# Performance work log

Measured on AMD Instinct MI355X. Metric: run time of the kernel, lower is better.

Reference implementation:

```python
import jax, jax.numpy as jnp
import numpy as np

N = 50000      # nodes
E = 1_600_000  # edges (avg degree 32)
G = 2000       # graphs in batch
H = 2          # attention heads
C = 64         # out_channels
IN = 64        # in_channels
NEG_SLOPE = 0.2


def setup_inputs() -> dict:
    key = jax.random.key(0)
    ks = jax.random.split(key, 6)
    x = jax.random.normal(ks[0], (N, IN), dtype=jnp.float32)
    edge_index = jax.random.randint(ks[1], (2, E), 0, N, dtype=jnp.int32)
    batch = jnp.sort(jax.random.randint(ks[2], (N,), 0, G, dtype=jnp.int32))
    # GATConv params: lin weight [H*C, IN] (glorot-ish), att vectors, bias [C]
    W = jax.random.normal(ks[3], (H * C, IN), dtype=jnp.float32) * (1.0 / np.sqrt(IN))
    att_src = jax.random.normal(ks[4], (1, H, C), dtype=jnp.float32) * 0.1
    att_dst = jax.random.normal(ks[5], (1, H, C), dtype=jnp.float32) * 0.1
    bias = jnp.zeros((C,), dtype=jnp.float32)
    return {"x": x, "edge_index": edge_index, "batch": batch,
            "W": W, "att_src": att_src, "att_dst": att_dst, "bias": bias}


def reference(x, edge_index, batch, W, att_src, att_dst, bias):
    # --- GATConv (PyG semantics: add_self_loops=True, concat=False -> head mean + bias) ---
    loops = jnp.arange(N, dtype=edge_index.dtype)
    src = jnp.concatenate([edge_index[0], loops])  # [E+N]
    dst = jnp.concatenate([edge_index[1], loops])  # [E+N]

    xp = (x @ W.T).reshape(N, H, C)                 # projected node feats [N,H,C]
    a_src = jnp.sum(xp * att_src, axis=-1)          # [N,H]
    a_dst = jnp.sum(xp * att_dst, axis=-1)          # [N,H]

    e = jax.nn.leaky_relu(a_src[src] + a_dst[dst], NEG_SLOPE)  # [E+N,H]
    # segment softmax over incoming edges of each destination node
    m = jax.ops.segment_max(e, dst, num_segments=N)            # [N,H]
    e = jnp.exp(e - m[dst])
    s = jax.ops.segment_sum(e, dst, num_segments=N)            # [N,H]
    alpha = e / s[dst]                                         # [E+N,H]

    msg = xp[src] * alpha[:, :, None]                          # [E+N,H,C]
    out = jax.ops.segment_sum(msg, dst, num_segments=N)        # [N,H,C]
    h_nodes = out.mean(axis=1) + bias                          # [N,C]

    # --- global_mean_pool ---
    sums = jax.ops.segment_sum(h_nodes, batch, num_segments=G)                     # [G,C]
    cnt = jax.ops.segment_sum(jnp.ones((N, 1), h_nodes.dtype), batch, num_segments=G)
    h_graphs = sums / jnp.maximum(cnt, 1.0)                                        # [G,C]
    return (h_nodes, h_graphs)
```

## Files before the change

### kernel.cpp

```cpp
#include <hip/hip_runtime.h>
#include <hip/hip_bf16.h>

#define H 2
#define C 64
#define IN_CH 64
#define HC (H*C)
#define NEG_SLOPE 0.2f
#define NBUCK_MAX 256
#define SBLK 512
#define CAP 12288

__global__ __launch_bounds__(128) void proj_kernel(
    const float* __restrict__ x, const float* __restrict__ W,
    const float* __restrict__ att_src, const float* __restrict__ att_dst,
    __hip_bfloat16* __restrict__ xp, float* __restrict__ asrc,
    float* __restrict__ adst, int* __restrict__ cnt, int N, int nbuck) {
    int t = threadIdx.x;
    if (blockIdx.x == 0)
        for (int i = t; i < nbuck; i += 128) cnt[i] = 0;
    float w[64];
    const float4* wr = reinterpret_cast<const float4*>(W + (size_t)t * IN_CH);
#pragma unroll
    for (int q = 0; q < 16; q++) {
        float4 v = wr[q];
        w[4 * q] = v.x; w[4 * q + 1] = v.y; w[4 * q + 2] = v.z; w[4 * q + 3] = v.w;
    }
    float a_s = att_src[t], a_d = att_dst[t];
    int lane = t & 63, head = t >> 6;
    for (int n = blockIdx.x; n < N; n += gridDim.x) {
        const float* xr = x + (size_t)n * IN_CH;
        float acc = 0.f;
#pragma unroll
        for (int k = 0; k < 64; k++) acc = fmaf(w[k], xr[k], acc);
        xp[(size_t)n * HC + t] = __float2bfloat16(acc);
        float as = acc * a_s, ad = acc * a_d;
#pragma unroll
        for (int d = 32; d > 0; d >>= 1) {
            as += __shfl_xor(as, d, 64);
            ad += __shfl_xor(ad, d, 64);
        }
        if (lane == 0) {
            asrc[(size_t)n * H + head] = as;
            adst[(size_t)n * H + head] = ad;
        }
    }
}

__global__ __launch_bounds__(256) void scatter_kernel(
    const int* __restrict__ edge, int* __restrict__ cnt,
    int* __restrict__ staged, int N, int E) {
    const int tid = threadIdx.x, bid = blockIdx.x;
    const int nbuck = (N + 255) >> 8;
    const int chunkE = (E + SBLK - 1) / SBLK;
    const int* srcE = edge;
    const int* dstE = edge + E;
    __shared__ int lh[NBUCK_MAX], bse[NBUCK_MAX], lcur[NBUCK_MAX];
    for (int i = tid; i < nbuck; i += 256) { lh[i] = 0; lcur[i] = 0; }
    __syncthreads();
    int beg = bid * chunkE, end = min(beg + chunkE, E);
    for (int i = beg + tid; i < end; i += 256)
        atomicAdd(&lh[dstE[i] >> 8], 1);
    __syncthreads();
    for (int i = tid; i < nbuck; i += 256) {
        int c = lh[i];
        bse[i] = (c > 0) ? atomicAdd(&cnt[i], c) : 0;
    }
    __syncthreads();
    for (int i = beg + tid; i < end; i += 256) {
        int s = srcE[i], d = dstE[i];
        int b = d >> 8;
        int l = atomicAdd(&lcur[b], 1);
        staged[(size_t)b * CAP + bse[b] + l] = s | ((d & 255) << 20);
    }
}

__global__ __launch_bounds__(512) void bucket_csr_kernel(
    const int* __restrict__ staged, const int* __restrict__ cnt,
    int* __restrict__ off, int* __restrict__ csr, int N, int nbuck) {
    int b = blockIdx.x, t = threadIdx.x;
    __shared__ int bse[256], rs[256], lh[256], sh[256], cur[256];
    {
        int v = (t < nbuck) ? cnt[t] : 0;
        if (t < 256) { bse[t] = v; rs[t] = v; }
        __syncthreads();
        for (int d = 1; d < 256; d <<= 1) {
            int u = (t >= d && t < 256) ? bse[t - d] : 0;
            __syncthreads();
            if (t < 256) bse[t] += u;
            __syncthreads();
        }
        if (t < 256) bse[t] -= rs[t];
        __syncthreads();
    }
    int base = bse[b], size = rs[b];
    const int* st = staged + (size_t)b * CAP;
    if (t < 256) lh[t] = 0;
    __syncthreads();
    for (int i = t; i < size; i += 512)
        atomicAdd(&lh[st[i] >> 20], 1);
    __syncthreads();
    int v = (t < 256) ? lh[t] : 0;
    if (t < 256) sh[t] = v;
    __syncthreads();
    for (int d = 1; d < 256; d <<= 1) {
        int u = (t >= d && t < 256) ? sh[t - d] : 0;
        __syncthreads();
        if (t < 256) sh[t] += u;
        __syncthreads();
    }
    if (t < 256) {
        int ex = sh[t] - v;
        int nd = b * 256 + t;
        if (nd < N) off[nd] = base + ex;
        if (nd == N - 1) off[N] = base + size;
        cur[t] = base + ex;
    }
    __syncthreads();
    for (int i = t; i < size; i += 512) {
        int e = st[i];
        int pos = atomicAdd(&cur[e >> 20], 1);
        csr[pos] = e & 0xFFFFF;
    }
}

template<int NB16>
__device__ __forceinline__ void gather_fma(const uint* __restrict__ xpw,
                                           const int* __restrict__ sidx,
                                           const float2* __restrict__ swt,
                                           int lane, float& accx, float& accy) {
    uint bu[NB16 * 16];
#pragma unroll
    for (int j = 0; j < NB16 * 16; j++) {
        int s2 = sidx[j];
        bu[j] = xpw[(size_t)s2 * 64 + lane];
    }
#pragma unroll
    for (int j = 0; j < NB16 * 16; j++) {
        float2 wv = swt[j];
        float wgt = (lane < 32) ? wv.x : wv.y;
        accx = fmaf(wgt, __uint_as_float(bu[j] << 16), accx);
        accy = fmaf(wgt, __uint_as_float(bu[j] & 0xffff0000u), accy);
    }
}

__global__ __launch_bounds__(256, 4) void aggregate_kernel(
    const __hip_bfloat16* __restrict__ xp, const float2* __restrict__ asrc,
    const float2* __restrict__ adst, const int* __restrict__ off,
    const int* __restrict__ csr, const float* __restrict__ bias,
    float* __restrict__ out, int N) {
    __shared__ int sidx[4][64];
    __shared__ float2 swt[4][64];
    int wid = threadIdx.x >> 6;
    int n = blockIdx.x * 4 + wid;
    if (n >= N) return;
    int lane = threadIdx.x & 63;
    int* si = sidx[wid];
    float2* sw = swt[wid];
    int o0 = off[n];
    int degE = off[n + 1] - o0;
    float2 ad = adst[n];
    float2 asn = asrc[n];
    float es0 = asn.x + ad.x; es0 = (es0 > 0.f) ? es0 : NEG_SLOPE * es0;
    float es1 = asn.y + ad.y; es1 = (es1 > 0.f) ? es1 : NEG_SLOPE * es1;
    float ws0 = __expf(es0), ws1 = __expf(es1);
    float s0 = (lane == 0) ? ws0 : 0.f;
    float s1 = (lane == 0) ? ws1 : 0.f;

    const uint* xpw = reinterpret_cast<const uint*>(xp);
    float accx, accy;
    {
        float wgt = (lane < 32) ? ws0 : ws1;
        uint u = xpw[(size_t)n * 64 + lane];
        accx = wgt * __uint_as_float(u << 16);
        accy = wgt * __uint_as_float(u & 0xffff0000u);
    }

    for (int base = 0; base < degE; base += 64) {
        int i = base + lane;
        int idx = 0;
        float w0 = 0.f, w1 = 0.f;
        if (i < degE) {
            idx = csr[o0 + i];
            float2 as = asrc[idx];
            float t0 = as.x + ad.x; t0 = (t0 > 0.f) ? t0 : NEG_SLOPE * t0;
            float t1 = as.y + ad.y; t1 = (t1 > 0.f) ? t1 : NEG_SLOPE * t1;
            w0 = __expf(t0);
            w1 = __expf(t1);
        }
        s0 += w0;
        s1 += w1;
        si[lane] = idx;
        sw[lane] = make_float2(w0, w1);
        int cnt2 = min(degE - base, 64);
        int nb16 = (cnt2 + 15) >> 4;
        switch (nb16) {
            case 1: gather_fma<1>(xpw, si, sw, lane, accx, accy); break;
            case 2: gather_fma<2>(xpw, si, sw, lane, accx, accy); break;
            case 3: gather_fma<3>(xpw, si, sw, lane, accx, accy); break;
            default: gather_fma<4>(xpw, si, sw, lane, accx, accy); break;
        }
    }
#pragma unroll
    for (int d = 32; d > 0; d >>= 1) {
        s0 += __shfl_xor(s0, d, 64);
        s1 += __shfl_xor(s1, d, 64);
    }
    float inv = (lane < 32) ? (1.f / s0) : (1.f / s1);
    accx *= inv;
    accy *= inv;
    float ox = 0.5f * (accx + __shfl_xor(accx, 32, 64));
    float oy = 0.5f * (accy + __shfl_xor(accy, 32, 64));
    if (lane < 32) {
        float vx = ox + bias[2 * lane];
        float vy = oy + bias[2 * lane + 1];
        *reinterpret_cast<float2*>(out + (size_t)n * C + 2 * lane) = make_float2(vx, vy);
    }
}

__global__ __launch_bounds__(256) void pool_kernel(const float* __restrict__ hn,
                                                   const int* __restrict__ batch,
                                                   float* __restrict__ outG, int N, int G) {
    int g = blockIdx.x;
    int c = threadIdx.x & 63, r = threadIdx.x >> 6;
    int lo = 0, hi = N;
    while (lo < hi) { int mid = (lo + hi) >> 1; if (batch[mid] < g) lo = mid + 1; else hi = mid; }
    int beg = lo;
    hi = N;
    while (lo < hi) { int mid = (lo + hi) >> 1; if (batch[mid] <= g) lo = mid + 1; else hi = mid; }
    int end = lo;
    float s = 0.f;
    for (int n = beg + r; n < end; n += 4) s += hn[(size_t)n * C + c];
    __shared__ float red[256];
    red[threadIdx.x] = s;
    __syncthreads();
    if (r == 0) {
        float tot = red[c] + red[64 + c] + red[128 + c] + red[192 + c];
        outG[(size_t)g * C + c] = tot / fmaxf((float)(end - beg), 1.f);
    }
}

extern "C" void kernel_launch(void* const* d_in, const int* in_sizes, int n_in,
                              void* d_out, int out_size, void* d_ws, size_t ws_size,
                              hipStream_t stream) {
    const float* x       = (const float*)d_in[0];
    const int*   edge    = (const int*)d_in[1];
    const int*   batch   = (const int*)d_in[2];
    const float* W       = (const float*)d_in[3];
    const float* att_src = (const float*)d_in[4];
    const float* att_dst = (const float*)d_in[5];
    const float* bias    = (const float*)d_in[6];

    int N = in_sizes[0] / IN_CH;
    int E = in_sizes[1] / 2;
    int G = out_size / C - N;
    int nbuck = (N + 255) >> 8;

    char* p = (char*)d_ws;
    auto alloc = [&](size_t bytes) {
        char* r = p;
        p += (bytes + 255) & ~(size_t)255;
        return r;
    };
    __hip_bfloat16* xp = (__hip_bfloat16*)alloc((size_t)N * HC * 2);
    float* asrc    = (float*)alloc((size_t)N * H * 4);
    float* adst    = (float*)alloc((size_t)N * H * 4);
    int*   cnt     = (int*)alloc((size_t)nbuck * 4);
    int*   off     = (int*)alloc((size_t)(N + 1) * 4);
    int*   staged  = (int*)alloc((size_t)nbuck * CAP * 4);
    int*   csr     = (int*)alloc((size_t)E * 4);

    proj_kernel<<<2048, 128, 0, stream>>>(x, W, att_src, att_dst, xp, asrc, adst,
                                          cnt, N, nbuck);
    scatter_kernel<<<SBLK, 256, 0, stream>>>(edge, cnt, staged, N, E);
    bucket_csr_kernel<<<nbuck, 512, 0, stream>>>(staged, cnt, off, csr, N, nbuck);
    aggregate_kernel<<<(N + 3) / 4, 256, 0, stream>>>(xp, (const float2*)asrc,
                                                      (const float2*)adst, off, csr, bias,
                                                      (float*)d_out, N);
    pool_kernel<<<G, 256, 0, stream>>>((const float*)d_out, batch,
                                       (float*)d_out + (size_t)N * C, N, G);
}
```

Before: 215.4 us.

## Fuse bucket CSR build into aggregation kernel using LDS-resident adjacency

Removes the separate bucket_csr kernel and the global off/csr arrays. Each aggregation block now reads one staged bucket, keeps only the destination nodes of its quarter, counting-sorts their sources into LDS and aggregates 64 nodes (16 per wave). This cuts a kernel launch and the global CSR write and read. In exchange each bucket's staged edges are read four times, and the grid shrinks to about 784 blocks of 256 threads with 16KB of LDS each, which may reduce occupancy and latency hiding for the gathers.

```diff
diff --git a/kernel.cpp b/kernel.cpp
--- a/kernel.cpp
+++ b/kernel.cpp
@@ -9,6 +9,7 @@
 #define NBUCK_MAX 256
 #define SBLK 512
 #define CAP 12288
+#define QCAP 4096
 
 __global__ __launch_bounds__(128) void proj_kernel(
     const float* __restrict__ x, const float* __restrict__ W,
@@ -74,55 +75,6 @@
     }
 }
 
-__global__ __launch_bounds__(512) void bucket_csr_kernel(
-    const int* __restrict__ staged, const int* __restrict__ cnt,
-    int* __restrict__ off, int* __restrict__ csr, int N, int nbuck) {
-    int b = blockIdx.x, t = threadIdx.x;
-    __shared__ int bse[256], rs[256], lh[256], sh[256], cur[256];
-    {
-        int v = (t < nbuck) ? cnt[t] : 0;
-        if (t < 256) { bse[t] = v; rs[t] = v; }
-        __syncthreads();
-        for (int d = 1; d < 256; d <<= 1) {
-            int u = (t >= d && t < 256) ? bse[t - d] : 0;
-            __syncthreads();
-            if (t < 256) bse[t] += u;
-            __syncthreads();
-        }
-        if (t < 256) bse[t] -= rs[t];
-        __syncthreads();
-    }
-    int base = bse[b], size = rs[b];
-    const int* st = staged + (size_t)b * CAP;
-    if (t < 256) lh[t] = 0;
-    __syncthreads();
-    for (int i = t; i < size; i += 512)
-        atomicAdd(&lh[st[i] >> 20], 1);
-    __syncthreads();
-    int v = (t < 256) ? lh[t] : 0;
-    if (t < 256) sh[t] = v;
-    __syncthreads();
-    for (int d = 1; d < 256; d <<= 1) {
-        int u = (t >= d && t < 256) ? sh[t - d] : 0;
-        __syncthreads();
-        if (t < 256) sh[t] += u;
-        __syncthreads();
-    }
-    if (t < 256) {
-        int ex = sh[t] - v;
-        int nd = b * 256 + t;
-        if (nd < N) off[nd] = base + ex;
-        if (nd == N - 1) off[N] = base + size;
-        cur[t] = base + ex;
-    }
-    __syncthreads();
-    for (int i = t; i < size; i += 512) {
-        int e = st[i];
-        int pos = atomicAdd(&cur[e >> 20], 1);
-        csr[pos] = e & 0xFFFFF;
-    }
-}
-
 template<int NB16>
 __device__ __forceinline__ void gather_fma(const uint* __restrict__ xpw,
                                            const int* __restrict__ sidx,
@@ -143,77 +95,115 @@
     }
 }
 
-__global__ __launch_bounds__(256, 4) void aggregate_kernel(
+__global__ __launch_bounds__(256, 4) void csr_aggregate_kernel(
+    const int* __restrict__ staged, const int* __restrict__ cnt,
     const __hip_bfloat16* __restrict__ xp, const float2* __restrict__ asrc,
-    const float2* __restrict__ adst, const int* __restrict__ off,
-    const int* __restrict__ csr, const float* __restrict__ bias,
+    const float2* __restrict__ adst, const float* __restrict__ bias,
     float* __restrict__ out, int N) {
-    __shared__ int sidx[4][64];
+    int b = blockIdx.x >> 2, q = blockIdx.x & 3;
+    int tid = threadIdx.x, lane = tid & 63, wid = tid >> 6;
+    __shared__ int lh[64], sc[64], cur[64];
+    __shared__ int ldsCsr[QCAP];
     __shared__ float2 swt[4][64];
-    int wid = threadIdx.x >> 6;
-    int n = blockIdx.x * 4 + wid;
-    if (n >= N) return;
-    int lane = threadIdx.x & 63;
-    int* si = sidx[wid];
-    float2* sw = swt[wid];
-    int o0 = off[n];
-    int degE = off[n + 1] - o0;
-    float2 ad = adst[n];
-    float2 asn = asrc[n];
-    float es0 = asn.x + ad.x; es0 = (es0 > 0.f) ? es0 : NEG_SLOPE * es0;
-    float es1 = asn.y + ad.y; es1 = (es1 > 0.f) ? es1 : NEG_SLOPE * es1;
-    float ws0 = __expf(es0), ws1 = __expf(es1);
-    float s0 = (lane == 0) ? ws0 : 0.f;
-    float s1 = (lane == 0) ? ws1 : 0.f;
+    int size = cnt[b];
+    const int* st = staged + (size_t)b * CAP;
+
+    if (tid < 64) lh[tid] = 0;
+    __syncthreads();
+    for (int i = tid; i < size; i += 256) {
+        int e = st[i];
+        int dl = e >> 20;
+        if ((dl >> 6) == q) atomicAdd(&lh[dl & 63], 1);
+    }
+    __syncthreads();
+    if (tid < 64) {
+        int v = lh[tid];
+        int incl = v;
+#pragma unroll
+        for (int d = 1; d < 64; d <<= 1) {
+            int u = __shfl_up(incl, d, 64);
+            if (lane >= d) incl += u;
+        }
+        sc[tid] = incl - v;
+        cur[tid] = incl - v;
+    }
+    __syncthreads();
+    int total = sc[63] + lh[63];
+    for (int i = tid; i < size; i += 256) {
+        int e = st[i];
+        int dl = e >> 20;
+        if ((dl >> 6) == q) {
+            int pos = atomicAdd(&cur[dl & 63], 1);
+            ldsCsr[pos] = e & 0xFFFFF;
+        }
+    }
+    __syncthreads();
+    if (tid < 80) {
+        int z = total + tid;
+        if (z < QCAP) ldsCsr[z] = 0;
+    }
+    __syncthreads();
 
     const uint* xpw = reinterpret_cast<const uint*>(xp);
-    float accx, accy;
-    {
-        float wgt = (lane < 32) ? ws0 : ws1;
-        uint u = xpw[(size_t)n * 64 + lane];
-        accx = wgt * __uint_as_float(u << 16);
-        accy = wgt * __uint_as_float(u & 0xffff0000u);
-    }
-
-    for (int base = 0; base < degE; base += 64) {
-        int i = base + lane;
-        int idx = 0;
-        float w0 = 0.f, w1 = 0.f;
-        if (i < degE) {
-            idx = csr[o0 + i];
-            float2 as = asrc[idx];
-            float t0 = as.x + ad.x; t0 = (t0 > 0.f) ? t0 : NEG_SLOPE * t0;
-            float t1 = as.y + ad.y; t1 = (t1 > 0.f) ? t1 : NEG_SLOPE * t1;
-            w0 = __expf(t0);
-            w1 = __expf(t1);
-        }
-        s0 += w0;
-        s1 += w1;
-        si[lane] = idx;
-        sw[lane] = make_float2(w0, w1);
-        int cnt2 = min(degE - base, 64);
-        int nb16 = (cnt2 + 15) >> 4;
-        switch (nb16) {
-            case 1: gather_fma<1>(xpw, si, sw, lane, accx, accy); break;
-            case 2: gather_fma<2>(xpw, si, sw, lane, accx, accy); break;
-            case 3: gather_fma<3>(xpw, si, sw, lane, accx, accy); break;
-            default: gather_fma<4>(xpw, si, sw, lane, accx, accy); break;
-        }
-    }
-#pragma unroll
-    for (int d = 32; d > 0; d >>= 1) {
-        s0 += __shfl_xor(s0, d, 64);
-        s1 += __shfl_xor(s1, d, 64);
-    }
-    float inv = (lane < 32) ? (1.f / s0) : (1.f / s1);
-    accx *= inv;
-    accy *= inv;
-    float ox = 0.5f * (accx + __shfl_xor(accx, 32, 64));
-    float oy = 0.5f * (accy + __shfl_xor(accy, 32, 64));
-    if (lane < 32) {
-        float vx = ox + bias[2 * lane];
-        float vy = oy + bias[2 * lane + 1];
-        *reinterpret_cast<float2*>(out + (size_t)n * C + 2 * lane) = make_float2(vx, vy);
+    for (int k = 0; k < 16; k++) {
+        int l = wid * 16 + k;
+        int n = b * 256 + q * 64 + l;
+        if (n >= N) break;
+        int o0 = sc[l];
+        int degE = lh[l];
+        float2 ad = adst[n];
+        float2 asn = asrc[n];
+        float es0 = asn.x + ad.x; es0 = (es0 > 0.f) ? es0 : NEG_SLOPE * es0;
+        float es1 = asn.y + ad.y; es1 = (es1 > 0.f) ? es1 : NEG_SLOPE * es1;
+        float ws0 = __expf(es0), ws1 = __expf(es1);
+        float s0 = (lane == 0) ? ws0 : 0.f;
+        float s1 = (lane == 0) ? ws1 : 0.f;
+        float accx, accy;
+        {
+            float wgt = (lane < 32) ? ws0 : ws1;
+            uint u = xpw[(size_t)n * 64 + lane];
+            accx = wgt * __uint_as_float(u << 16);
+            accy = wgt * __uint_as_float(u & 0xffff0000u);
+        }
+        for (int base = 0; base < degE; base += 64) {
+            int i = base + lane;
+            float w0 = 0.f, w1 = 0.f;
+            if (i < degE) {
+                int idx = ldsCsr[o0 + i];
+                float2 as = asrc[idx];
+                float t0 = as.x + ad.x; t0 = (t0 > 0.f) ? t0 : NEG_SLOPE * t0;
+                float t1 = as.y + ad.y; t1 = (t1 > 0.f) ? t1 : NEG_SLOPE * t1;
+                w0 = __expf(t0);
+                w1 = __expf(t1);
+            }
+            s0 += w0;
+            s1 += w1;
+            swt[wid][lane] = make_float2(w0, w1);
+            int cnt2 = min(degE - base, 64);
+            int nb16 = (cnt2 + 15) >> 4;
+            const int* sidx = ldsCsr + o0 + base;
+            switch (nb16) {
+                case 1: gather_fma<1>(xpw, sidx, swt[wid], lane, accx, accy); break;
+                case 2: gather_fma<2>(xpw, sidx, swt[wid], lane, accx, accy); break;
+                case 3: gather_fma<3>(xpw, sidx, swt[wid], lane, accx, accy); break;
+                default: gather_fma<4>(xpw, sidx, swt[wid], lane, accx, accy); break;
+            }
+        }
+#pragma unroll
+        for (int d = 32; d > 0; d >>= 1) {
+            s0 += __shfl_xor(s0, d, 64);
+            s1 += __shfl_xor(s1, d, 64);
+        }
+        float inv = (lane < 32) ? (1.f / s0) : (1.f / s1);
+        accx *= inv;
+        accy *= inv;
+        float ox = 0.5f * (accx + __shfl_xor(accx, 32, 64));
+        float oy = 0.5f * (accy + __shfl_xor(accy, 32, 64));
+        if (lane < 32) {
+            float vx = ox + bias[2 * lane];
+            float vy = oy + bias[2 * lane + 1];
+            *reinterpret_cast<float2*>(out + (size_t)n * C + 2 * lane) = make_float2(vx, vy);
+        }
     }
 }
 
@@ -265,17 +255,15 @@
     float* asrc    = (float*)alloc((size_t)N * H * 4);
     float* adst    = (float*)alloc((size_t)N * H * 4);
     int*   cnt     = (int*)alloc((size_t)nbuck * 4);
-    int*   off     = (int*)alloc((size_t)(N + 1) * 4);
     int*   staged  = (int*)alloc((size_t)nbuck * CAP * 4);
-    int*   csr     = (int*)alloc((size_t)E * 4);
 
     proj_kernel<<<2048, 128, 0, stream>>>(x, W, att_src, att_dst, xp, asrc, adst,
                                           cnt, N, nbuck);
     scatter_kernel<<<SBLK, 256, 0, stream>>>(edge, cnt, staged, N, E);
-    bucket_csr_kernel<<<nbuck, 512, 0, stream>>>(staged, cnt, off, csr, N, nbuck);
-    aggregate_kernel<<<(N + 3) / 4, 256, 0, stream>>>(xp, (const float2*)asrc,
-                                                      (const float2*)adst, off, csr, bias,
-                                                      (float*)d_out, N);
+    csr_aggregate_kernel<<<nbuck * 4, 256, 0, stream>>>(staged, cnt, xp,
+                                                        (const float2*)asrc,
+                                                        (const float2*)adst, bias,
+                                                        (float*)d_out, N);
     pool_kernel<<<G, 256, 0, stream>>>((const float*)d_out, batch,
                                        (float*)d_out + (size_t)N * C, N, G);
 }
```

New measurement: 223.3 us. 3.7% more time.

## Precompute edge attention weights and softmax denominators in CSR build kernel

Applied to the files above, without the earlier changes.

Moves the per-edge leaky-relu/exp weight computation and the per-node softmax denominator out of the aggregate kernel into the CSR construction kernel, where they are written to new wts and den arrays using shared-memory atomics. The aggregate kernel then loads precomputed weights instead of gathering asrc and recomputing exp, and drops its final shuffle reduction. The gather unroll granularity also changes from 16 to 8 edges to cut wasted loads on partial chunks. The cost is an extra 8 bytes per edge written and read back, plus float atomics in shared memory in the CSR kernel.

```diff
diff --git a/kernel.cpp b/kernel.cpp
--- a/kernel.cpp
+++ b/kernel.cpp
@@ -74,11 +74,15 @@
     }
 }
 
-__global__ __launch_bounds__(512) void bucket_csr_kernel(
+__global__ __launch_bounds__(512) void csr_weights_kernel(
     const int* __restrict__ staged, const int* __restrict__ cnt,
-    int* __restrict__ off, int* __restrict__ csr, int N, int nbuck) {
+    const float2* __restrict__ asrc, const float2* __restrict__ adst,
+    int* __restrict__ off, int* __restrict__ csr, float2* __restrict__ wts,
+    float2* __restrict__ den, int N, int nbuck) {
     int b = blockIdx.x, t = threadIdx.x;
     __shared__ int bse[256], rs[256], lh[256], sh[256], cur[256];
+    __shared__ float2 adL[256];
+    __shared__ float denS[512];
     {
         int v = (t < nbuck) ? cnt[t] : 0;
         if (t < 256) { bse[t] = v; rs[t] = v; }
@@ -94,7 +98,23 @@
     }
     int base = bse[b], size = rs[b];
     const int* st = staged + (size_t)b * CAP;
-    if (t < 256) lh[t] = 0;
+    if (t < 256) {
+        lh[t] = 0;
+        int nd = b * 256 + t;
+        if (nd < N) {
+            float2 ad = adst[nd];
+            adL[t] = ad;
+            float2 asn = asrc[nd];
+            float e0 = asn.x + ad.x; e0 = (e0 > 0.f) ? e0 : NEG_SLOPE * e0;
+            float e1 = asn.y + ad.y; e1 = (e1 > 0.f) ? e1 : NEG_SLOPE * e1;
+            denS[2 * t] = __expf(e0);
+            denS[2 * t + 1] = __expf(e1);
+        } else {
+            adL[t] = make_float2(0.f, 0.f);
+            denS[2 * t] = 1.f;
+            denS[2 * t + 1] = 1.f;
+        }
+    }
     __syncthreads();
     for (int i = t; i < size; i += 512)
         atomicAdd(&lh[st[i] >> 20], 1);
@@ -118,24 +138,38 @@
     __syncthreads();
     for (int i = t; i < size; i += 512) {
         int e = st[i];
-        int pos = atomicAdd(&cur[e >> 20], 1);
-        csr[pos] = e & 0xFFFFF;
-    }
-}
-
-template<int NB16>
+        int s = e & 0xFFFFF, dl = e >> 20;
+        float2 as = asrc[s];
+        float2 ad = adL[dl];
+        float e0 = as.x + ad.x; e0 = (e0 > 0.f) ? e0 : NEG_SLOPE * e0;
+        float e1 = as.y + ad.y; e1 = (e1 > 0.f) ? e1 : NEG_SLOPE * e1;
+        float w0 = __expf(e0), w1 = __expf(e1);
+        int pos = atomicAdd(&cur[dl], 1);
+        csr[pos] = s;
+        wts[pos] = make_float2(w0, w1);
+        atomicAdd(&denS[2 * dl], w0);
+        atomicAdd(&denS[2 * dl + 1], w1);
+    }
+    __syncthreads();
+    if (t < 256) {
+        int nd = b * 256 + t;
+        if (nd < N) den[nd] = make_float2(denS[2 * t], denS[2 * t + 1]);
+    }
+}
+
+template<int NB>
 __device__ __forceinline__ void gather_fma(const uint* __restrict__ xpw,
                                            const int* __restrict__ sidx,
                                            const float2* __restrict__ swt,
                                            int lane, float& accx, float& accy) {
-    uint bu[NB16 * 16];
-#pragma unroll
-    for (int j = 0; j < NB16 * 16; j++) {
+    uint bu[NB * 8];
+#pragma unroll
+    for (int j = 0; j < NB * 8; j++) {
         int s2 = sidx[j];
         bu[j] = xpw[(size_t)s2 * 64 + lane];
     }
 #pragma unroll
-    for (int j = 0; j < NB16 * 16; j++) {
+    for (int j = 0; j < NB * 8; j++) {
         float2 wv = swt[j];
         float wgt = (lane < 32) ? wv.x : wv.y;
         accx = fmaf(wgt, __uint_as_float(bu[j] << 16), accx);
@@ -146,7 +180,8 @@
 __global__ __launch_bounds__(256, 4) void aggregate_kernel(
     const __hip_bfloat16* __restrict__ xp, const float2* __restrict__ asrc,
     const float2* __restrict__ adst, const int* __restrict__ off,
-    const int* __restrict__ csr, const float* __restrict__ bias,
+    const int* __restrict__ csr, const float2* __restrict__ wts,
+    const float2* __restrict__ den, const float* __restrict__ bias,
     float* __restrict__ out, int N) {
     __shared__ int sidx[4][64];
     __shared__ float2 swt[4][64];
@@ -158,13 +193,12 @@
     float2* sw = swt[wid];
     int o0 = off[n];
     int degE = off[n + 1] - o0;
+    float2 dn = den[n];
     float2 ad = adst[n];
     float2 asn = asrc[n];
     float es0 = asn.x + ad.x; es0 = (es0 > 0.f) ? es0 : NEG_SLOPE * es0;
     float es1 = asn.y + ad.y; es1 = (es1 > 0.f) ? es1 : NEG_SLOPE * es1;
     float ws0 = __expf(es0), ws1 = __expf(es1);
-    float s0 = (lane == 0) ? ws0 : 0.f;
-    float s1 = (lane == 0) ? ws1 : 0.f;
 
     const uint* xpw = reinterpret_cast<const uint*>(xp);
     float accx, accy;
@@ -178,34 +212,27 @@
     for (int base = 0; base < degE; base += 64) {
         int i = base + lane;
         int idx = 0;
-        float w0 = 0.f, w1 = 0.f;
+        float2 w2 = make_float2(0.f, 0.f);
         if (i < degE) {
             idx = csr[o0 + i];
-            float2 as = asrc[idx];
-            float t0 = as.x + ad.x; t0 = (t0 > 0.f) ? t0 : NEG_SLOPE * t0;
-            float t1 = as.y + ad.y; t1 = (t1 > 0.f) ? t1 : NEG_SLOPE * t1;
-            w0 = __expf(t0);
-            w1 = __expf(t1);
-        }
-        s0 += w0;
-        s1 += w1;
+            w2 = wts[o0 + i];
+        }
         si[lane] = idx;
-        sw[lane] = make_float2(w0, w1);
+        sw[lane] = w2;
         int cnt2 = min(degE - base, 64);
-        int nb16 = (cnt2 + 15) >> 4;
-        switch (nb16) {
+        int nb8 = (cnt2 + 7) >> 3;
+        switch (nb8) {
             case 1: gather_fma<1>(xpw, si, sw, lane, accx, accy); break;
             case 2: gather_fma<2>(xpw, si, sw, lane, accx, accy); break;
             case 3: gather_fma<3>(xpw, si, sw, lane, accx, accy); break;
-            default: gather_fma<4>(xpw, si, sw, lane, accx, accy); break;
-        }
-    }
-#pragma unroll
-    for (int d = 32; d > 0; d >>= 1) {
-        s0 += __shfl_xor(s0, d, 64);
-        s1 += __shfl_xor(s1, d, 64);
-    }
-    float inv = (lane < 32) ? (1.f / s0) : (1.f / s1);
+            case 4: gather_fma<4>(xpw, si, sw, lane, accx, accy); break;
+            case 5: gather_fma<5>(xpw, si, sw, lane, accx, accy); break;
+            case 6: gather_fma<6>(xpw, si, sw, lane, accx, accy); break;
+            case 7: gather_fma<7>(xpw, si, sw, lane, accx, accy); break;
+            default: gather_fma<8>(xpw, si, sw, lane, accx, accy); break;
+        }
+    }
+    float inv = (lane < 32) ? (1.f / dn.x) : (1.f / dn.y);
     accx *= inv;
     accy *= inv;
     float ox = 0.5f * (accx + __shfl_xor(accx, 32, 64));
@@ -268,14 +295,18 @@
     int*   off     = (int*)alloc((size_t)(N + 1) * 4);
     int*   staged  = (int*)alloc((size_t)nbuck * CAP * 4);
     int*   csr     = (int*)alloc((size_t)E * 4);
+    float2* wts    = (float2*)alloc((size_t)E * 8);
+    float2* den    = (float2*)alloc((size_t)N * 8);
 
     proj_kernel<<<2048, 128, 0, stream>>>(x, W, att_src, att_dst, xp, asrc, adst,
                                           cnt, N, nbuck);
     scatter_kernel<<<SBLK, 256, 0, stream>>>(edge, cnt, staged, N, E);
-    bucket_csr_kernel<<<nbuck, 512, 0, stream>>>(staged, cnt, off, csr, N, nbuck);
+    csr_weights_kernel<<<nbuck, 512, 0, stream>>>(staged, cnt, (const float2*)asrc,
+                                                  (const float2*)adst, off, csr, wts, den,
+                                                  N, nbuck);
     aggregate_kernel<<<(N + 3) / 4, 256, 0, stream>>>(xp, (const float2*)asrc,
-                                                      (const float2*)adst, off, csr, bias,
-                                                      (float*)d_out, N);
+                                                      (const float2*)adst, off, csr, wts, den,
+                                                      bias, (float*)d_out, N);
     pool_kernel<<<G, 256, 0, stream>>>((const float*)d_out, batch,
                                        (float*)d_out + (size_t)N * C, N, G);
 }
```

After: 226.7 us. +5.3%, slower.

## Fuse mean-pool into aggregation via atomics, shrink buckets, cache edges in LDS

Applied to the files above, without the earlier changes.

The per-graph mean pool now happens inside the aggregation kernel. Each node atomically adds its output row into per-graph sums and counts, and a small finalize kernel divides. This removes the separate pool kernel that re-read node outputs after a binary search. The CSR build uses 128-node buckets instead of 256, which means more bucket blocks with smaller per-bucket scans. The scatter kernel caches its edge chunk in LDS so edges are read from global memory only once. The cost is many float atomics on hot graph rows, plus float-sum ordering that is no longer deterministic.

```diff
diff --git a/kernel.cpp b/kernel.cpp
--- a/kernel.cpp
+++ b/kernel.cpp
@@ -6,18 +6,25 @@
 #define IN_CH 64
 #define HC (H*C)
 #define NEG_SLOPE 0.2f
-#define NBUCK_MAX 256
+#define NBUCK_MAX 512
 #define SBLK 512
-#define CAP 12288
+#define CHUNK_MAX 3136
+#define CAP 6144
 
 __global__ __launch_bounds__(128) void proj_kernel(
     const float* __restrict__ x, const float* __restrict__ W,
     const float* __restrict__ att_src, const float* __restrict__ att_dst,
     __hip_bfloat16* __restrict__ xp, float* __restrict__ asrc,
-    float* __restrict__ adst, int* __restrict__ cnt, int N, int nbuck) {
+    float* __restrict__ adst, int* __restrict__ cnt, float* __restrict__ gsum,
+    int* __restrict__ gcnt, int N, int nbuck, int G) {
     int t = threadIdx.x;
-    if (blockIdx.x == 0)
+    if (blockIdx.x < 64) {
+        for (int i = blockIdx.x * 128 + t; i < G * C; i += 64 * 128) gsum[i] = 0.f;
+    } else if (blockIdx.x == 64) {
+        for (int i = t; i < G; i += 128) gcnt[i] = 0;
+    } else if (blockIdx.x == 65) {
         for (int i = t; i < nbuck; i += 128) cnt[i] = 0;
+    }
     float w[64];
     const float4* wr = reinterpret_cast<const float4*>(W + (size_t)t * IN_CH);
 #pragma unroll
@@ -50,27 +57,30 @@
     const int* __restrict__ edge, int* __restrict__ cnt,
     int* __restrict__ staged, int N, int E) {
     const int tid = threadIdx.x, bid = blockIdx.x;
-    const int nbuck = (N + 255) >> 8;
+    const int nbuck = (N + 127) >> 7;
     const int chunkE = (E + SBLK - 1) / SBLK;
     const int* srcE = edge;
     const int* dstE = edge + E;
+    __shared__ int2 eds[CHUNK_MAX];
     __shared__ int lh[NBUCK_MAX], bse[NBUCK_MAX], lcur[NBUCK_MAX];
     for (int i = tid; i < nbuck; i += 256) { lh[i] = 0; lcur[i] = 0; }
     __syncthreads();
     int beg = bid * chunkE, end = min(beg + chunkE, E);
-    for (int i = beg + tid; i < end; i += 256)
-        atomicAdd(&lh[dstE[i] >> 8], 1);
-    __syncthreads();
-    for (int i = tid; i < nbuck; i += 256) {
-        int c = lh[i];
-        bse[i] = (c > 0) ? atomicAdd(&cnt[i], c) : 0;
-    }
-    __syncthreads();
-    for (int i = beg + tid; i < end; i += 256) {
-        int s = srcE[i], d = dstE[i];
-        int b = d >> 8;
+    int m = end - beg;
+    for (int i = tid; i < m; i += 256) {
+        int s = srcE[beg + i], d = dstE[beg + i];
+        eds[i] = make_int2(s, d);
+        atomicAdd(&lh[d >> 7], 1);
+    }
+    __syncthreads();
+    for (int i = tid; i < nbuck; i += 256)
+        bse[i] = atomicAdd(&cnt[i], lh[i]);
+    __syncthreads();
+    for (int i = tid; i < m; i += 256) {
+        int2 e = eds[i];
+        int b = e.y >> 7;
         int l = atomicAdd(&lcur[b], 1);
-        staged[(size_t)b * CAP + bse[b] + l] = s | ((d & 255) << 20);
+        staged[(size_t)b * CAP + bse[b] + l] = e.x | ((e.y & 127) << 20);
     }
 }
 
@@ -78,39 +88,39 @@
     const int* __restrict__ staged, const int* __restrict__ cnt,
     int* __restrict__ off, int* __restrict__ csr, int N, int nbuck) {
     int b = blockIdx.x, t = threadIdx.x;
-    __shared__ int bse[256], rs[256], lh[256], sh[256], cur[256];
+    __shared__ int bse[512], rs[512], lh[128], sh[128], cur[128];
     {
         int v = (t < nbuck) ? cnt[t] : 0;
-        if (t < 256) { bse[t] = v; rs[t] = v; }
-        __syncthreads();
-        for (int d = 1; d < 256; d <<= 1) {
-            int u = (t >= d && t < 256) ? bse[t - d] : 0;
+        bse[t] = v; rs[t] = v;
+        __syncthreads();
+        for (int d = 1; d < 512; d <<= 1) {
+            int u = (t >= d) ? bse[t - d] : 0;
             __syncthreads();
-            if (t < 256) bse[t] += u;
+            bse[t] += u;
             __syncthreads();
         }
-        if (t < 256) bse[t] -= rs[t];
+        bse[t] -= rs[t];
         __syncthreads();
     }
     int base = bse[b], size = rs[b];
     const int* st = staged + (size_t)b * CAP;
-    if (t < 256) lh[t] = 0;
+    if (t < 128) lh[t] = 0;
     __syncthreads();
     for (int i = t; i < size; i += 512)
         atomicAdd(&lh[st[i] >> 20], 1);
     __syncthreads();
-    int v = (t < 256) ? lh[t] : 0;
-    if (t < 256) sh[t] = v;
-    __syncthreads();
-    for (int d = 1; d < 256; d <<= 1) {
-        int u = (t >= d && t < 256) ? sh[t - d] : 0;
-        __syncthreads();
-        if (t < 256) sh[t] += u;
-        __syncthreads();
-    }
-    if (t < 256) {
+    int v = (t < 128) ? lh[t] : 0;
+    if (t < 128) sh[t] = v;
+    __syncthreads();
+    for (int d = 1; d < 128; d <<= 1) {
+        int u = (t >= d && t < 128) ? sh[t - d] : 0;
+        __syncthreads();
+        if (t < 128) sh[t] += u;
+        __syncthreads();
+    }
+    if (t < 128) {
         int ex = sh[t] - v;
-        int nd = b * 256 + t;
+        int nd = b * 128 + t;
         if (nd < N) off[nd] = base + ex;
         if (nd == N - 1) off[N] = base + size;
         cur[t] = base + ex;
@@ -147,7 +157,8 @@
     const __hip_bfloat16* __restrict__ xp, const float2* __restrict__ asrc,
     const float2* __restrict__ adst, const int* __restrict__ off,
     const int* __restrict__ csr, const float* __restrict__ bias,
-    float* __restrict__ out, int N) {
+    const int* __restrict__ batch, float* __restrict__ out,
+    float* __restrict__ gsum, int* __restrict__ gcnt, int N) {
     __shared__ int sidx[4][64];
     __shared__ float2 swt[4][64];
     int wid = threadIdx.x >> 6;
@@ -210,33 +221,24 @@
     accy *= inv;
     float ox = 0.5f * (accx + __shfl_xor(accx, 32, 64));
     float oy = 0.5f * (accy + __shfl_xor(accy, 32, 64));
+    int g = batch[n];
     if (lane < 32) {
         float vx = ox + bias[2 * lane];
         float vy = oy + bias[2 * lane + 1];
         *reinterpret_cast<float2*>(out + (size_t)n * C + 2 * lane) = make_float2(vx, vy);
-    }
-}
-
-__global__ __launch_bounds__(256) void pool_kernel(const float* __restrict__ hn,
-                                                   const int* __restrict__ batch,
-                                                   float* __restrict__ outG, int N, int G) {
-    int g = blockIdx.x;
-    int c = threadIdx.x & 63, r = threadIdx.x >> 6;
-    int lo = 0, hi = N;
-    while (lo < hi) { int mid = (lo + hi) >> 1; if (batch[mid] < g) lo = mid + 1; else hi = mid; }
-    int beg = lo;
-    hi = N;
-    while (lo < hi) { int mid = (lo + hi) >> 1; if (batch[mid] <= g) lo = mid + 1; else hi = mid; }
-    int end = lo;
-    float s = 0.f;
-    for (int n = beg + r; n < end; n += 4) s += hn[(size_t)n * C + c];
-    __shared__ float red[256];
-    red[threadIdx.x] = s;
-    __syncthreads();
-    if (r == 0) {
-        float tot = red[c] + red[64 + c] + red[128 + c] + red[192 + c];
-        outG[(size_t)g * C + c] = tot / fmaxf((float)(end - beg), 1.f);
-    }
+        atomicAdd(&gsum[(size_t)g * C + 2 * lane], vx);
+        atomicAdd(&gsum[(size_t)g * C + 2 * lane + 1], vy);
+    }
+    if (lane == 0) atomicAdd(&gcnt[g], 1);
+}
+
+__global__ __launch_bounds__(256) void finalize_kernel(const float* __restrict__ gsum,
+                                                       const int* __restrict__ gcnt,
+                                                       float* __restrict__ outG, int G) {
+    int i = blockIdx.x * 256 + threadIdx.x;
+    if (i >= G * C) return;
+    int g = i >> 6;
+    outG[i] = gsum[i] / fmaxf((float)max(gcnt[g], 1), 1.f);
 }
 
 extern "C" void kernel_launch(void* const* d_in, const int* in_sizes, int n_in,
@@ -253,7 +255,7 @@
     int N = in_sizes[0] / IN_CH;
     int E = in_sizes[1] / 2;
     int G = out_size / C - N;
-    int nbuck = (N + 255) >> 8;
+    int nbuck = (N + 127) >> 7;
 
     char* p = (char*)d_ws;
     auto alloc = [&](size_t bytes) {
@@ -268,14 +270,16 @@
     int*   off     = (int*)alloc((size_t)(N + 1) * 4);
     int*   staged  = (int*)alloc((size_t)nbuck * CAP * 4);
     int*   csr     = (int*)alloc((size_t)E * 4);
+    float* gsum    = (float*)alloc((size_t)G * C * 4);
+    int*   gcnt    = (int*)alloc((size_t)G * 4);
 
     proj_kernel<<<2048, 128, 0, stream>>>(x, W, att_src, att_dst, xp, asrc, adst,
-                                          cnt, N, nbuck);
+                                          cnt, gsum, gcnt, N, nbuck, G);
     scatter_kernel<<<SBLK, 256, 0, stream>>>(edge, cnt, staged, N, E);
     bucket_csr_kernel<<<nbuck, 512, 0, stream>>>(staged, cnt, off, csr, N, nbuck);
     aggregate_kernel<<<(N + 3) / 4, 256, 0, stream>>>(xp, (const float2*)asrc,
                                                       (const float2*)adst, off, csr, bias,
-                                                      (float*)d_out, N);
-    pool_kernel<<<G, 256, 0, stream>>>((const float*)d_out, batch,
-                                       (float*)d_out + (size_t)N * C, N, G);
-}
+                                                      batch, (float*)d_out, gsum, gcnt, N);
+    finalize_kernel<<<(G * C + 255) / 256, 256, 0, stream>>>(gsum, gcnt,
+                                                             (float*)d_out + (size_t)N * C, G);
+}
```

Result: slower. 230.0 us (+6.8%).
